# Kernel optimization log

Hardware: AMD Instinct MI355X
Metric: run time of the kernel (lower is better)

Reference implementation:

```python
import jax, jax.numpy as jnp
import numpy as np

NUM_EXPERTS_TOTAL = 9  # 8 routed + 1 shared (shared expert is also routed via softmax in this module)
TOP_K = 2


def setup_inputs() -> dict:
    key = jax.random.key(0)
    k0, k1, k2, k3, k4 = jax.random.split(key, 5)
    B, S, H, I = 2, 2048, 1024, 2816
    E = NUM_EXPERTS_TOTAL
    x = jax.random.normal(k0, (B, S, H), dtype=jnp.float32)
    Wr = (jax.random.normal(k1, (H, E), dtype=jnp.float32) * 0.02)          # router (no bias)
    Wg = (jax.random.normal(k2, (E, H, I), dtype=jnp.float32) * 0.02)       # gate_proj per expert
    Wu = (jax.random.normal(k3, (E, H, I), dtype=jnp.float32) * 0.02)       # up_proj per expert
    Wd = (jax.random.normal(k4, (E, I, H), dtype=jnp.float32) * 0.02)       # down_proj per expert
    return {"x": x, "Wr": Wr, "Wg": Wg, "Wu": Wu, "Wd": Wd}


def reference(x, Wr, Wg, Wu, Wd):
    B, S, H = x.shape
    E = NUM_EXPERTS_TOTAL
    T = B * S

    # Router: softmax over all 9 experts, then top-2 and renormalize
    logits = jnp.einsum('bsh,he->bse', x, Wr)
    probs = jax.nn.softmax(logits, axis=-1)
    topk_w, topk_idx = jax.lax.top_k(probs, TOP_K)                 # [B,S,K]
    topk_w = topk_w / jnp.sum(topk_w, axis=-1, keepdims=True)

    xf = x.reshape(T, H)
    wf = topk_w.reshape(T, TOP_K)
    idxf = topk_idx.reshape(T, TOP_K)

    # Per-token combine weight for each expert (0 if not selected)
    cw = jnp.zeros((T, E), dtype=x.dtype).at[jnp.arange(T)[:, None], idxf].add(wf)  # [T,E]

    # SwiGLU MLP for every expert (tokens with cw==0 contribute nothing)
    gate = jax.nn.silu(jnp.einsum('th,ehi->tei', xf, Wg))          # [T,E,I]
    hidden = gate * jnp.einsum('th,ehi->tei', xf, Wu)              # [T,E,I]
    out = jnp.einsum('tei,eih,te->th', hidden, Wd, cw)             # weighted combine
    return out.reshape(B, S, H)
```

## Files before the change

kernel.cpp:

```cpp
#include <hip/hip_runtime.h>
#include <cstdint>
#include <cstddef>

#define T_TOK 4096
#define H_DIM 1024
#define I_DIM 2816
#define E_NUM 9
#define MAXTILE 76

typedef __bf16 bf16;
typedef bf16 bf16x4 __attribute__((ext_vector_type(4)));
typedef bf16 bf16x8 __attribute__((ext_vector_type(8)));
typedef float f32x4 __attribute__((ext_vector_type(4)));

constexpr int BM = 128, BN = 128, BK = 32;
constexpr int HTILE = BM * BK;

#define GL16(gp, lp)                                                                   \
  __builtin_amdgcn_global_load_lds((const __attribute__((address_space(1))) void*)(gp), \
                                   (__attribute__((address_space(3))) void*)(lp), 16, 0, 0)

__global__ __launch_bounds__(256) void k_xcast(const float* __restrict__ x, bf16* __restrict__ xb) {
  size_t i = ((size_t)blockIdx.x * 256 + threadIdx.x) * 8;
  float4 a = *reinterpret_cast<const float4*>(x + i);
  float4 b = *reinterpret_cast<const float4*>(x + i + 4);
  bf16x8 v;
  v[0]=(bf16)a.x; v[1]=(bf16)a.y; v[2]=(bf16)a.z; v[3]=(bf16)a.w;
  v[4]=(bf16)b.x; v[5]=(bf16)b.y; v[6]=(bf16)b.z; v[7]=(bf16)b.w;
  *reinterpret_cast<bf16x8*>(xb + i) = v;
}

__global__ __launch_bounds__(256) void k_transpose(const float* __restrict__ in,
                                                   bf16* __restrict__ out, int R, int C) {
  const float* src = in + (size_t)blockIdx.z * R * C;
  bf16* dst = out + (size_t)blockIdx.z * R * C;
  __shared__ bf16 tile[64][68];
  int r0 = blockIdx.y * 64, c0 = blockIdx.x * 64;
  int t = threadIdx.x;
  int tr = t >> 4, tc = (t & 15) * 4;
#pragma unroll
  for (int it = 0; it < 4; ++it) {
    int r = tr + it * 16;
    float4 v = *reinterpret_cast<const float4*>(src + (size_t)(r0 + r) * C + c0 + tc);
    bf16x4 w; w[0]=(bf16)v.x; w[1]=(bf16)v.y; w[2]=(bf16)v.z; w[3]=(bf16)v.w;
    *reinterpret_cast<bf16x4*>(&tile[r][tc]) = w;
  }
  __syncthreads();
#pragma unroll
  for (int it = 0; it < 4; ++it) {
    int oc = tr + it * 16;
    bf16x4 w;
    w[0] = tile[tc + 0][oc]; w[1] = tile[tc + 1][oc];
    w[2] = tile[tc + 2][oc]; w[3] = tile[tc + 3][oc];
    *reinterpret_cast<bf16x4*>(dst + (size_t)(c0 + oc) * R + r0 + tc) = w;
  }
}

__global__ __launch_bounds__(256) void k_router(const float* __restrict__ x,
                                                const float* __restrict__ Wr,
                                                int* __restrict__ ridx,
                                                float* __restrict__ rw,
                                                int* __restrict__ counts) {
  int lane = threadIdx.x & 63;
  int wid  = threadIdx.x >> 6;
  int t = blockIdx.x * 4 + wid;
  const float* xr = x + (size_t)t * H_DIM;
  float acc[E_NUM];
#pragma unroll
  for (int e = 0; e < E_NUM; ++e) acc[e] = 0.f;
  for (int h = lane; h < H_DIM; h += 64) {
    float xv = xr[h];
    const float* wr = Wr + h * E_NUM;
#pragma unroll
    for (int e = 0; e < E_NUM; ++e) acc[e] += xv * wr[e];
  }
#pragma unroll
  for (int off = 32; off > 0; off >>= 1) {
#pragma unroll
    for (int e = 0; e < E_NUM; ++e) acc[e] += __shfl_xor(acc[e], off);
  }
  if (lane == 0) {
    int i0 = 0;
#pragma unroll
    for (int e = 1; e < E_NUM; ++e) if (acc[e] > acc[i0]) i0 = e;
    int i1 = (i0 == 0) ? 1 : 0;
#pragma unroll
    for (int e = 0; e < E_NUM; ++e) if (e != i0 && acc[e] > acc[i1]) i1 = e;
    float r  = expf(acc[i1] - acc[i0]);
    float w0 = 1.f / (1.f + r);
    float w1 = r / (1.f + r);
    ridx[2 * t]     = i0;
    ridx[2 * t + 1] = i1;
    rw[2 * t]     = w0;
    rw[2 * t + 1] = w1;
    atomicAdd(&counts[i0], 1);
    atomicAdd(&counts[i1], 1);
  }
}

__global__ void k_scan(const int* __restrict__ counts, int* __restrict__ offsets,
                       int* __restrict__ cursor, int* __restrict__ tiles,
                       int* __restrict__ n_tiles) {
  if (threadIdx.x == 0) {
    int s = 0, nt = 0;
    for (int e = 0; e < E_NUM; ++e) {
      offsets[e] = s;
      int c = counts[e];
      for (int pt = 0; pt * BM < c && nt < MAXTILE; ++pt) tiles[nt++] = (e << 16) | pt;
      s += c;
    }
    offsets[E_NUM] = s;
    *n_tiles = nt;
  }
  if (threadIdx.x < E_NUM) cursor[threadIdx.x] = 0;
}

__global__ __launch_bounds__(256) void k_scatter(const int* __restrict__ ridx,
                                                 const int* __restrict__ offsets,
                                                 int* __restrict__ cursor,
                                                 int* __restrict__ perm) {
  int t = blockIdx.x * 256 + threadIdx.x;
  if (t >= T_TOK) return;
#pragma unroll
  for (int k = 0; k < 2; ++k) {
    int e = ridx[2 * t + k];
    int pos = atomicAdd(&cursor[e], 1);
    perm[offsets[e] + pos] = 2 * t + k;
  }
}

__global__ __launch_bounds__(256, 2) void k_gateup(const bf16* __restrict__ xb,
                                                   const bf16* __restrict__ WgT,
                                                   const bf16* __restrict__ WuT,
                                                   const int* __restrict__ perm,
                                                   const int* __restrict__ offsets,
                                                   const int* __restrict__ tiles,
                                                   const int* __restrict__ n_tiles,
                                                   bf16* __restrict__ hidden) {
  if ((int)blockIdx.y >= *n_tiles) return;
  int tv = tiles[blockIdx.y];
  int e = tv >> 16, pt = tv & 0xffff;
  int seg0 = offsets[e], cnt = offsets[e + 1] - seg0;
  int n0 = blockIdx.x * BN;

  __shared__ bf16 As[2 * HTILE];
  __shared__ bf16 Bg[2 * HTILE];
  __shared__ bf16 Bu[2 * HTILE];

  int tid = threadIdx.x, lane = tid & 63, wid = tid >> 6;
  int wm = wid >> 1, wn = wid & 1, l15 = lane & 15, l16 = lane >> 4;

  int srow1 = tid >> 2, srow2 = 64 + srow1;
  int kc = (tid & 3) * 8;
  int p1 = pt * BM + srow1, p2 = pt * BM + srow2;
  const bf16* a1 = xb + (size_t)(perm[seg0 + (p1 < cnt ? p1 : 0)] >> 1) * H_DIM + kc;
  const bf16* a2 = xb + (size_t)(perm[seg0 + (p2 < cnt ? p2 : 0)] >> 1) * H_DIM + kc;
  const bf16* g1 = WgT + ((size_t)e * I_DIM + n0 + srow1) * H_DIM + kc;
  const bf16* g2 = WgT + ((size_t)e * I_DIM + n0 + srow2) * H_DIM + kc;
  const bf16* u1 = WuT + ((size_t)e * I_DIM + n0 + srow1) * H_DIM + kc;
  const bf16* u2 = WuT + ((size_t)e * I_DIM + n0 + srow2) * H_DIM + kc;
  bf16* lA1 = &As[tid * 8];       bf16* lA2 = &As[2048 + tid * 8];
  bf16* lG1 = &Bg[tid * 8];       bf16* lG2 = &Bg[2048 + tid * 8];
  bf16* lU1 = &Bu[tid * 8];       bf16* lU2 = &Bu[2048 + tid * 8];

  f32x4 accg[4][4], accu[4][4];
#pragma unroll
  for (int m = 0; m < 4; ++m)
#pragma unroll
    for (int n = 0; n < 4; ++n) {
      accg[m][n] = (f32x4){0.f, 0.f, 0.f, 0.f};
      accu[m][n] = (f32x4){0.f, 0.f, 0.f, 0.f};
    }

  for (int k0 = 0; k0 < H_DIM; k0 += 2 * BK) {
    GL16(a1 + k0, lA1);            GL16(a2 + k0, lA2);
    GL16(a1 + k0 + BK, lA1 + HTILE); GL16(a2 + k0 + BK, lA2 + HTILE);
    GL16(g1 + k0, lG1);            GL16(g2 + k0, lG2);
    GL16(g1 + k0 + BK, lG1 + HTILE); GL16(g2 + k0 + BK, lG2 + HTILE);
    GL16(u1 + k0, lU1);            GL16(u2 + k0, lU2);
    GL16(u1 + k0 + BK, lU1 + HTILE); GL16(u2 + k0 + BK, lU2 + HTILE);
    __syncthreads();

#pragma unroll
    for (int kk = 0; kk < 2; ++kk) {
      const bf16* Ab = &As[kk * HTILE];
      const bf16* Gb = &Bg[kk * HTILE];
      const bf16* Ub = &Bu[kk * HTILE];
      bf16x8 af[4], bg[4], bu[4];
#pragma unroll
      for (int m = 0; m < 4; ++m)
        af[m] = *reinterpret_cast<const bf16x8*>(&Ab[(wm * 64 + m * 16 + l15) * BK + l16 * 8]);
#pragma unroll
      for (int n = 0; n < 4; ++n) {
        bg[n] = *reinterpret_cast<const bf16x8*>(&Gb[(wn * 64 + n * 16 + l15) * BK + l16 * 8]);
        bu[n] = *reinterpret_cast<const bf16x8*>(&Ub[(wn * 64 + n * 16 + l15) * BK + l16 * 8]);
      }
#pragma unroll
      for (int m = 0; m < 4; ++m)
#pragma unroll
        for (int n = 0; n < 4; ++n) {
          accg[m][n] = __builtin_amdgcn_mfma_f32_16x16x32_bf16(af[m], bg[n], accg[m][n], 0, 0, 0);
          accu[m][n] = __builtin_amdgcn_mfma_f32_16x16x32_bf16(af[m], bu[n], accu[m][n], 0, 0, 0);
        }
    }
    __syncthreads();
  }

#pragma unroll
  for (int m = 0; m < 4; ++m) {
#pragma unroll
    for (int r = 0; r < 4; ++r) {
      int p_glob = pt * BM + wm * 64 + m * 16 + l16 * 4 + r;
      if (p_glob < cnt) {
        bf16* hrow = hidden + (size_t)(seg0 + p_glob) * I_DIM;
#pragma unroll
        for (int n = 0; n < 4; ++n) {
          int col = n0 + wn * 64 + n * 16 + l15;
          float g = accg[m][n][r];
          float u = accu[m][n][r];
          float h = g / (1.f + __expf(-g)) * u;
          hrow[col] = (bf16)h;
        }
      }
    }
  }
}

__global__ __launch_bounds__(256, 2) void k_down(const bf16* __restrict__ hidden,
                                                 const bf16* __restrict__ WdT,
                                                 const int* __restrict__ perm,
                                                 const int* __restrict__ offsets,
                                                 const int* __restrict__ tiles,
                                                 const int* __restrict__ n_tiles,
                                                 float* __restrict__ pair_out) {
  if ((int)blockIdx.y >= *n_tiles) return;
  int tv = tiles[blockIdx.y];
  int e = tv >> 16, pt = tv & 0xffff;
  int seg0 = offsets[e], cnt = offsets[e + 1] - seg0;
  int n0 = blockIdx.x * BN;

  __shared__ bf16 As[2 * HTILE];
  __shared__ bf16 Bs[2 * HTILE];

  int tid = threadIdx.x, lane = tid & 63, wid = tid >> 6;
  int wm = wid >> 1, wn = wid & 1, l15 = lane & 15, l16 = lane >> 4;

  int srow1 = tid >> 2, srow2 = 64 + srow1;
  int kc = (tid & 3) * 8;
  int p1 = pt * BM + srow1, p2 = pt * BM + srow2;
  const bf16* a1 = hidden + (size_t)(seg0 + (p1 < cnt ? p1 : 0)) * I_DIM + kc;
  const bf16* a2 = hidden + (size_t)(seg0 + (p2 < cnt ? p2 : 0)) * I_DIM + kc;
  const bf16* b1 = WdT + ((size_t)e * H_DIM + n0 + srow1) * I_DIM + kc;
  const bf16* b2 = WdT + ((size_t)e * H_DIM + n0 + srow2) * I_DIM + kc;
  bf16* lA1 = &As[tid * 8];  bf16* lA2 = &As[2048 + tid * 8];
  bf16* lB1 = &Bs[tid * 8];  bf16* lB2 = &Bs[2048 + tid * 8];

  f32x4 acc[4][4];
#pragma unroll
  for (int m = 0; m < 4; ++m)
#pragma unroll
    for (int n = 0; n < 4; ++n) acc[m][n] = (f32x4){0.f, 0.f, 0.f, 0.f};

  for (int k0 = 0; k0 < I_DIM; k0 += 2 * BK) {
    GL16(a1 + k0, lA1);            GL16(a2 + k0, lA2);
    GL16(a1 + k0 + BK, lA1 + HTILE); GL16(a2 + k0 + BK, lA2 + HTILE);
    GL16(b1 + k0, lB1);            GL16(b2 + k0, lB2);
    GL16(b1 + k0 + BK, lB1 + HTILE); GL16(b2 + k0 + BK, lB2 + HTILE);
    __syncthreads();

#pragma unroll
    for (int kk = 0; kk < 2; ++kk) {
      const bf16* Ab = &As[kk * HTILE];
      const bf16* Bb = &Bs[kk * HTILE];
      bf16x8 af[4], bfr[4];
#pragma unroll
      for (int m = 0; m < 4; ++m)
        af[m] = *reinterpret_cast<const bf16x8*>(&Ab[(wm * 64 + m * 16 + l15) * BK + l16 * 8]);
#pragma unroll
      for (int n = 0; n < 4; ++n)
        bfr[n] = *reinterpret_cast<const bf16x8*>(&Bb[(wn * 64 + n * 16 + l15) * BK + l16 * 8]);
#pragma unroll
      for (int m = 0; m < 4; ++m)
#pragma unroll
        for (int n = 0; n < 4; ++n)
          acc[m][n] = __builtin_amdgcn_mfma_f32_16x16x32_bf16(af[m], bfr[n], acc[m][n], 0, 0, 0);
    }
    __syncthreads();
  }

#pragma unroll
  for (int m = 0; m < 4; ++m) {
#pragma unroll
    for (int r = 0; r < 4; ++r) {
      int p_glob = pt * BM + wm * 64 + m * 16 + l16 * 4 + r;
      if (p_glob < cnt) {
        int pair = perm[seg0 + p_glob];
        float* orow = pair_out + (size_t)pair * H_DIM;
#pragma unroll
        for (int n = 0; n < 4; ++n) {
          int col = n0 + wn * 64 + n * 16 + l15;
          orow[col] = acc[m][n][r];
        }
      }
    }
  }
}

__global__ __launch_bounds__(256) void k_combine(const float* __restrict__ pair_out,
                                                 const float* __restrict__ rw,
                                                 float* __restrict__ out) {
  int t = blockIdx.x;
  int c = threadIdx.x;
  float w0 = rw[2 * t];
  float w1 = rw[2 * t + 1];
  float4 a = *reinterpret_cast<const float4*>(pair_out + ((size_t)(2 * t)) * H_DIM + c * 4);
  float4 b = *reinterpret_cast<const float4*>(pair_out + ((size_t)(2 * t + 1)) * H_DIM + c * 4);
  float4 o;
  o.x = w0 * a.x + w1 * b.x;
  o.y = w0 * a.y + w1 * b.y;
  o.z = w0 * a.z + w1 * b.z;
  o.w = w0 * a.w + w1 * b.w;
  *reinterpret_cast<float4*>(out + (size_t)t * H_DIM + c * 4) = o;
}

extern "C" void kernel_launch(void* const* d_in, const int* in_sizes, int n_in,
                              void* d_out, int out_size, void* d_ws, size_t ws_size,
                              hipStream_t stream) {
  const float* x  = (const float*)d_in[0];
  const float* Wr = (const float*)d_in[1];
  const float* Wg = (const float*)d_in[2];
  const float* Wu = (const float*)d_in[3];
  const float* Wd = (const float*)d_in[4];
  float* out = (float*)d_out;

  char* ws = (char*)d_ws;
  int*   counts  = (int*)(ws);
  int*   cursor  = (int*)(ws + 256);
  int*   offsets = (int*)(ws + 512);
  int*   n_tiles = (int*)(ws + 768);
  int*   tiles   = (int*)(ws + 1024);
  int*   ridx    = (int*)(ws + 64 * 1024);
  float* rw      = (float*)(ws + 128 * 1024);
  int*   perm    = (int*)(ws + 192 * 1024);
  bf16*  xb      = (bf16*)(ws + (1ull << 20));
  bf16*  WgT     = (bf16*)(ws + (16ull << 20));
  bf16*  WuT     = (bf16*)(ws + (66ull << 20));
  bf16*  WdT     = (bf16*)(ws + (116ull << 20));
  bf16*  hidden  = (bf16*)(ws + (166ull << 20));
  float* pair_out = (float*)(ws + (212ull << 20));

  hipMemsetAsync(counts, 0, 64, stream);
  k_xcast<<<dim3(T_TOK * H_DIM / 2048), dim3(256), 0, stream>>>(x, xb);
  k_transpose<<<dim3(I_DIM / 64, H_DIM / 64, E_NUM), dim3(256), 0, stream>>>(Wg, WgT, H_DIM, I_DIM);
  k_transpose<<<dim3(I_DIM / 64, H_DIM / 64, E_NUM), dim3(256), 0, stream>>>(Wu, WuT, H_DIM, I_DIM);
  k_transpose<<<dim3(H_DIM / 64, I_DIM / 64, E_NUM), dim3(256), 0, stream>>>(Wd, WdT, I_DIM, H_DIM);
  k_router<<<dim3(T_TOK / 4), dim3(256), 0, stream>>>(x, Wr, ridx, rw, counts);
  k_scan<<<dim3(1), dim3(64), 0, stream>>>(counts, offsets, cursor, tiles, n_tiles);
  k_scatter<<<dim3((T_TOK + 255) / 256), dim3(256), 0, stream>>>(ridx, offsets, cursor, perm);
  k_gateup<<<dim3(I_DIM / BN, MAXTILE), dim3(256), 0, stream>>>(
      xb, WgT, WuT, perm, offsets, tiles, n_tiles, hidden);
  k_down<<<dim3(H_DIM / BN, MAXTILE), dim3(256), 0, stream>>>(
      hidden, WdT, perm, offsets, tiles, n_tiles, pair_out);
  k_combine<<<dim3(T_TOK), dim3(256), 0, stream>>>(pair_out, rw, out);
}
```

Before: 474.0 us.

## Split-K the down projection, store partials in bf16, swizzle gate/up grid for XCDs

The down-projection GEMM is split into two K halves over a third grid dimension. This doubles the number of blocks, since the original grid of 8 x n_tiles was small for the device, and each half writes bf16 partials. The combine kernel sums the two partials before applying the routing weights. The gate/up kernel now uses a flattened 1D grid whose block index is remapped so that consecutive blocks on each of the 8 XCDs share the same token tile, aiming for better L2 reuse. Rounding the partials to bf16 adds some precision loss.

```diff
diff --git a/kernel.cpp b/kernel.cpp
--- a/kernel.cpp
+++ b/kernel.cpp
@@ -7,6 +7,9 @@
 #define I_DIM 2816
 #define E_NUM 9
 #define MAXTILE 76
+#define NPANEL (I_DIM / 128)
+#define GUGRID (NPANEL * MAXTILE)
+#define GUCHUNK (GUGRID / 8)
 
 typedef __bf16 bf16;
 typedef bf16 bf16x4 __attribute__((ext_vector_type(4)));
@@ -137,11 +140,14 @@
                                                    const int* __restrict__ tiles,
                                                    const int* __restrict__ n_tiles,
                                                    bf16* __restrict__ hidden) {
-  if ((int)blockIdx.y >= *n_tiles) return;
-  int tv = tiles[blockIdx.y];
+  int flat = blockIdx.x;
+  int swz = (flat & 7) * GUCHUNK + (flat >> 3);
+  int ti = swz / NPANEL;
+  int n0 = (swz % NPANEL) * BN;
+  if (ti >= *n_tiles) return;
+  int tv = tiles[ti];
   int e = tv >> 16, pt = tv & 0xffff;
   int seg0 = offsets[e], cnt = offsets[e + 1] - seg0;
-  int n0 = blockIdx.x * BN;
 
   __shared__ bf16 As[2 * HTILE];
   __shared__ bf16 Bg[2 * HTILE];
@@ -232,12 +238,14 @@
                                                  const int* __restrict__ offsets,
                                                  const int* __restrict__ tiles,
                                                  const int* __restrict__ n_tiles,
-                                                 float* __restrict__ pair_out) {
+                                                 bf16* __restrict__ pair_half) {
   if ((int)blockIdx.y >= *n_tiles) return;
   int tv = tiles[blockIdx.y];
   int e = tv >> 16, pt = tv & 0xffff;
   int seg0 = offsets[e], cnt = offsets[e + 1] - seg0;
   int n0 = blockIdx.x * BN;
+  int kz = blockIdx.z * (I_DIM / 2);
+  bf16* pout = pair_half + (size_t)blockIdx.z * 2 * T_TOK * H_DIM;
 
   __shared__ bf16 As[2 * HTILE];
   __shared__ bf16 Bs[2 * HTILE];
@@ -248,10 +256,10 @@
   int srow1 = tid >> 2, srow2 = 64 + srow1;
   int kc = (tid & 3) * 8;
   int p1 = pt * BM + srow1, p2 = pt * BM + srow2;
-  const bf16* a1 = hidden + (size_t)(seg0 + (p1 < cnt ? p1 : 0)) * I_DIM + kc;
-  const bf16* a2 = hidden + (size_t)(seg0 + (p2 < cnt ? p2 : 0)) * I_DIM + kc;
-  const bf16* b1 = WdT + ((size_t)e * H_DIM + n0 + srow1) * I_DIM + kc;
-  const bf16* b2 = WdT + ((size_t)e * H_DIM + n0 + srow2) * I_DIM + kc;
+  const bf16* a1 = hidden + (size_t)(seg0 + (p1 < cnt ? p1 : 0)) * I_DIM + kz + kc;
+  const bf16* a2 = hidden + (size_t)(seg0 + (p2 < cnt ? p2 : 0)) * I_DIM + kz + kc;
+  const bf16* b1 = WdT + ((size_t)e * H_DIM + n0 + srow1) * I_DIM + kz + kc;
+  const bf16* b2 = WdT + ((size_t)e * H_DIM + n0 + srow2) * I_DIM + kz + kc;
   bf16* lA1 = &As[tid * 8];  bf16* lA2 = &As[2048 + tid * 8];
   bf16* lB1 = &Bs[tid * 8];  bf16* lB2 = &Bs[2048 + tid * 8];
 
@@ -261,7 +269,7 @@
 #pragma unroll
     for (int n = 0; n < 4; ++n) acc[m][n] = (f32x4){0.f, 0.f, 0.f, 0.f};
 
-  for (int k0 = 0; k0 < I_DIM; k0 += 2 * BK) {
+  for (int k0 = 0; k0 < I_DIM / 2; k0 += 2 * BK) {
     GL16(a1 + k0, lA1);            GL16(a2 + k0, lA2);
     GL16(a1 + k0 + BK, lA1 + HTILE); GL16(a2 + k0 + BK, lA2 + HTILE);
     GL16(b1 + k0, lB1);            GL16(b2 + k0, lB2);
@@ -295,31 +303,37 @@
       int p_glob = pt * BM + wm * 64 + m * 16 + l16 * 4 + r;
       if (p_glob < cnt) {
         int pair = perm[seg0 + p_glob];
-        float* orow = pair_out + (size_t)pair * H_DIM;
+        bf16* orow = pout + (size_t)pair * H_DIM;
 #pragma unroll
         for (int n = 0; n < 4; ++n) {
           int col = n0 + wn * 64 + n * 16 + l15;
-          orow[col] = acc[m][n][r];
+          orow[col] = (bf16)acc[m][n][r];
         }
       }
     }
   }
 }
 
-__global__ __launch_bounds__(256) void k_combine(const float* __restrict__ pair_out,
+__global__ __launch_bounds__(256) void k_combine(const bf16* __restrict__ pair_half,
                                                  const float* __restrict__ rw,
                                                  float* __restrict__ out) {
   int t = blockIdx.x;
   int c = threadIdx.x;
+  const bf16* z0 = pair_half;
+  const bf16* z1 = pair_half + (size_t)2 * T_TOK * H_DIM;
   float w0 = rw[2 * t];
   float w1 = rw[2 * t + 1];
-  float4 a = *reinterpret_cast<const float4*>(pair_out + ((size_t)(2 * t)) * H_DIM + c * 4);
-  float4 b = *reinterpret_cast<const float4*>(pair_out + ((size_t)(2 * t + 1)) * H_DIM + c * 4);
+  size_t r0 = (size_t)(2 * t) * H_DIM + c * 4;
+  size_t r1 = (size_t)(2 * t + 1) * H_DIM + c * 4;
+  bf16x4 a0 = *reinterpret_cast<const bf16x4*>(z0 + r0);
+  bf16x4 a1 = *reinterpret_cast<const bf16x4*>(z1 + r0);
+  bf16x4 b0 = *reinterpret_cast<const bf16x4*>(z0 + r1);
+  bf16x4 b1 = *reinterpret_cast<const bf16x4*>(z1 + r1);
   float4 o;
-  o.x = w0 * a.x + w1 * b.x;
-  o.y = w0 * a.y + w1 * b.y;
-  o.z = w0 * a.z + w1 * b.z;
-  o.w = w0 * a.w + w1 * b.w;
+  o.x = w0 * ((float)a0[0] + (float)a1[0]) + w1 * ((float)b0[0] + (float)b1[0]);
+  o.y = w0 * ((float)a0[1] + (float)a1[1]) + w1 * ((float)b0[1] + (float)b1[1]);
+  o.z = w0 * ((float)a0[2] + (float)a1[2]) + w1 * ((float)b0[2] + (float)b1[2]);
+  o.w = w0 * ((float)a0[3] + (float)a1[3]) + w1 * ((float)b0[3] + (float)b1[3]);
   *reinterpret_cast<float4*>(out + (size_t)t * H_DIM + c * 4) = o;
 }
 
@@ -347,7 +361,7 @@
   bf16*  WuT     = (bf16*)(ws + (66ull << 20));
   bf16*  WdT     = (bf16*)(ws + (116ull << 20));
   bf16*  hidden  = (bf16*)(ws + (166ull << 20));
-  float* pair_out = (float*)(ws + (212ull << 20));
+  bf16*  pair_half = (bf16*)(ws + (212ull << 20));
 
   hipMemsetAsync(counts, 0, 64, stream);
   k_xcast<<<dim3(T_TOK * H_DIM / 2048), dim3(256), 0, stream>>>(x, xb);
@@ -357,9 +371,9 @@
   k_router<<<dim3(T_TOK / 4), dim3(256), 0, stream>>>(x, Wr, ridx, rw, counts);
   k_scan<<<dim3(1), dim3(64), 0, stream>>>(counts, offsets, cursor, tiles, n_tiles);
   k_scatter<<<dim3((T_TOK + 255) / 256), dim3(256), 0, stream>>>(ridx, offsets, cursor, perm);
-  k_gateup<<<dim3(I_DIM / BN, MAXTILE), dim3(256), 0, stream>>>(
+  k_gateup<<<dim3(GUGRID), dim3(256), 0, stream>>>(
       xb, WgT, WuT, perm, offsets, tiles, n_tiles, hidden);
-  k_down<<<dim3(H_DIM / BN, MAXTILE), dim3(256), 0, stream>>>(
-      hidden, WdT, perm, offsets, tiles, n_tiles, pair_out);
-  k_combine<<<dim3(T_TOK), dim3(256), 0, stream>>>(pair_out, rw, out);
-}
+  k_down<<<dim3(H_DIM / BN, MAXTILE, 2), dim3(256), 0, stream>>>(
+      hidden, WdT, perm, offsets, tiles, n_tiles, pair_half);
+  k_combine<<<dim3(T_TOK), dim3(256), 0, stream>>>(pair_half, rw, out);
+}
```

New measurement: 473.8 us. About the same (-0.0%).
